# Optimization experiments

Hardware: AMD Instinct MI355X
Metric: run time of the kernel (lower is better)

The kernel has to match this reference:

```python
import jax, jax.numpy as jnp
import numpy as np

N_WORD, N_TOPIC, N_DOC = 30000, 1000, 15000
D_WORD, D_TOPIC, D_OUT = 300, 300, 128
E = dict(ww=800000, wt=400000, wd=600000, td=300000, tt=150000)
SRC_N = dict(ww=N_WORD, wt=N_WORD, wd=N_WORD, td=N_TOPIC, tt=N_TOPIC)
DST_N = dict(ww=N_WORD, wt=N_TOPIC, wd=N_DOC, td=N_DOC, tt=N_TOPIC)


def setup_inputs() -> dict:
    key = jax.random.key(0)
    ks = iter(jax.random.split(key, 64))
    inp = {}
    inp["feat_word"] = jax.random.normal(next(ks), (N_WORD, D_WORD), jnp.float32)
    inp["feat_topic"] = jax.random.normal(next(ks), (N_TOPIC, D_TOPIC), jnp.float32)
    for et in ["ww", "wt", "wd", "td", "tt"]:
        inp[f"{et}_src"] = jax.random.randint(next(ks), (E[et],), 0, SRC_N[et], jnp.int32)
        inp[f"{et}_dst"] = jax.random.randint(next(ks), (E[et],), 0, DST_N[et], jnp.int32)
        inp[f"{et}_w"] = jax.random.uniform(next(ks), (E[et],), jnp.float32)
        din = D_WORD if et[0] == "w" else D_TOPIC
        inp[f"W_{et}"] = jax.random.normal(next(ks), (din, D_OUT), jnp.float32) / np.float32(np.sqrt(din))
        inp[f"b_{et}"] = jnp.zeros((D_OUT,), jnp.float32)
    return inp


def _mean_agg(Wh, src, dst, w, n_dst):
    # DGL fn.u_mul_e('Wh','weight','m') + fn.mean('m','h'): per-edge message
    # Wh[src] * w, mean-reduced per destination node (0 for isolated nodes).
    m = Wh[src] * w[:, None]                                   # [E, D_OUT]
    s = jax.ops.segment_sum(m, dst, num_segments=n_dst)        # [n_dst, D_OUT]
    c = jax.ops.segment_sum(jnp.ones_like(w), dst, num_segments=n_dst)
    return s / jnp.maximum(c, 1.0)[:, None]


def reference(feat_word, feat_topic,
              ww_src, ww_dst, ww_w, wt_src, wt_dst, wt_w,
              wd_src, wd_dst, wd_w, td_src, td_dst, td_w,
              tt_src, tt_dst, tt_w,
              W_ww, b_ww, W_wt, b_wt, W_wd, b_wd, W_td, b_td, W_tt, b_tt):
    # NOTE: the original forward's causal/noise branch is dead code --
    # `Wh = self.weight[etype](feat_dict[srctype])` overwrites it, so the
    # live math is a plain per-edge-type linear projection of source feats.
    Wh_ww = feat_word @ W_ww + b_ww
    Wh_wt = feat_word @ W_wt + b_wt
    Wh_wd = feat_word @ W_wd + b_wd
    Wh_td = feat_topic @ W_td + b_td
    Wh_tt = feat_topic @ W_tt + b_tt
    # multi_update_all(..., 'sum'): sum the per-etype means per dst node type.
    h_word = _mean_agg(Wh_ww, ww_src, ww_dst, ww_w, N_WORD)
    h_topic = (_mean_agg(Wh_wt, wt_src, wt_dst, wt_w, N_TOPIC)
               + _mean_agg(Wh_tt, tt_src, tt_dst, tt_w, N_TOPIC))
    h_doc = (_mean_agg(Wh_wd, wd_src, wd_dst, wd_w, N_DOC)
             + _mean_agg(Wh_td, td_src, td_dst, td_w, N_DOC))
    return (h_word, h_topic, h_doc)
```

## Files before the change

kernel.cpp:

```cpp
#include <hip/hip_runtime.h>

#define N_WORD 30000
#define N_TOPIC 1000
#define N_DOC 15000
#define DIN 300
#define KP 320
#define DOUT 128

#define E_WW 800000
#define E_WT 400000
#define E_WD 600000
#define E_TD 300000
#define E_TT 150000

#define CC_WW 0
#define CC_WT 30000
#define CC_WD 31000
#define CC_TD 46000
#define CC_TT 61000
#define NBINS 62000

#define CAP_WW 80
#define CAP_WT 544
#define CAP_WD 96
#define CAP_TD 56
#define CAP_TT 240
#define SB_WW 0
#define SB_WT (SB_WW + N_WORD * CAP_WW)
#define SB_WD (SB_WT + N_TOPIC * CAP_WT)
#define SB_TD (SB_WD + N_DOC * CAP_WD)
#define SB_TT (SB_TD + N_DOC * CAP_TD)
#define SLOT_TOTAL (SB_TT + N_TOPIC * CAP_TT)

#define CNT_BLOCKS 360
#define HIST_TOTAL 4168000

#define CVT_W_CHUNKS 1200000
#define CVT_T_CHUNKS 40000
#define CVT_BLOCKS 1211
#define PREPW_BLOCKS 200

#define PFX_BLOCKS 244
#define GW_BLOCKS 469
#define GT_BLOCKS 16

#define CPAD 392

#define GB_TOPIC 250
#define GB_DOC 3750
#define GB_WORD 7500

using half8  = __attribute__((ext_vector_type(8))) _Float16;
using half2v = __attribute__((ext_vector_type(2))) _Float16;
using f32x4  = __attribute__((ext_vector_type(4))) float;

struct SegP {
    const int* src[5];
    const int* dst[5];
    const float* w[5];
};

struct WPtrs {
    const float* W[5];
    const float* b[5];
};

__device__ __forceinline__ void decode_grp(
    int b, int& ti, int& hx, int& dlo, int& bins, int& hb,
    int& ch, int& ne, int& cap, int& sbase)
{
    if (b < 64)       { ti=0; hx=b;     dlo=0;     bins=15000; hb=0;       ch=12500; ne=E_WW; cap=CAP_WW; sbase=SB_WW; }
    else if (b < 128) { ti=0; hx=b-64;  dlo=15000; bins=15000; hb=960000;  ch=12500; ne=E_WW; cap=CAP_WW; sbase=SB_WW; }
    else if (b < 192) { ti=1; hx=b-128; dlo=0;     bins=1000;  hb=1920000; ch=6250;  ne=E_WT; cap=CAP_WT; sbase=SB_WT; }
    else if (b < 288) { ti=2; hx=b-192; dlo=0;     bins=15000; hb=1984000; ch=6250;  ne=E_WD; cap=CAP_WD; sbase=SB_WD; }
    else if (b < 336) { ti=3; hx=b-288; dlo=0;     bins=15000; hb=3424000; ch=6250;  ne=E_TD; cap=CAP_TD; sbase=SB_TD; }
    else              { ti=4; hx=b-336; dlo=0;     bins=1000;  hb=4144000; ch=6250;  ne=E_TT; cap=CAP_TT; sbase=SB_TT; }
}

__device__ __forceinline__ void decode_pfx(
    int b, int& hb, int& bins, int& H, int& cb, int& tile)
{
    if (b < 59)       { hb=0;       bins=15000; H=64; cb=0;     tile=b; }
    else if (b < 118) { hb=960000;  bins=15000; H=64; cb=15000; tile=b-59; }
    else if (b < 122) { hb=1920000; bins=1000;  H=64; cb=30000; tile=b-118; }
    else if (b < 181) { hb=1984000; bins=15000; H=96; cb=31000; tile=b-122; }
    else if (b < 240) { hb=3424000; bins=15000; H=48; cb=46000; tile=b-181; }
    else              { hb=4144000; bins=1000;  H=24; cb=61000; tile=b-240; }
}

__global__ __launch_bounds__(1024) void prep_count(
    SegP S, unsigned short* __restrict__ hist,
    WPtrs WP, _Float16* __restrict__ Wt_word, _Float16* __restrict__ Wt_topic,
    float* __restrict__ bcat_word, float* __restrict__ bcat_topic,
    const float* __restrict__ feat_word, const float* __restrict__ feat_topic,
    _Float16* __restrict__ A16w, _Float16* __restrict__ A16t)
{
    __shared__ int h[15000];
    const int b = blockIdx.x;
    if (b < CNT_BLOCKS) {
        int ti, hx, dlo, bins, hb, ch, ne, cap, sbase;
        decode_grp(b, ti, hx, dlo, bins, hb, ch, ne, cap, sbase);
        (void)cap; (void)sbase;
        for (int i = threadIdx.x; i < bins; i += 1024) h[i] = 0;
        __syncthreads();
        const int* __restrict__ dst = S.dst[ti];
        int lo = hx * ch;
        int hiE = lo + ch; if (hiE > ne) hiE = ne;
        for (int i = lo + (int)threadIdx.x; i < hiE; i += 1024) {
            int ld = dst[i] - dlo;
            if ((unsigned)ld < (unsigned)bins) atomicAdd(&h[ld], 1);
        }
        __syncthreads();
        unsigned short* __restrict__ out = hist + hb + hx * bins;
        for (int i = threadIdx.x; i < bins; i += 1024)
            out[i] = (unsigned short)h[i];
    } else if (b < CNT_BLOCKS + CVT_BLOCKS) {
        int c = (b - CNT_BLOCKS) * 1024 + (int)threadIdx.x;
        if (c >= CVT_W_CHUNKS + CVT_T_CHUNKS) return;
        const float* src;
        _Float16* dstp;
        int row, k8;
        if (c < CVT_W_CHUNKS) { row = c / 40; k8 = c - row * 40; src = feat_word; dstp = A16w; }
        else { c -= CVT_W_CHUNKS; row = c / 40; k8 = c - row * 40; src = feat_topic; dstp = A16t; }
        int k = k8 * 8;
        const float* ap = src + (size_t)row * DIN + k;
        half8 hv = half8{0, 0, 0, 0, 0, 0, 0, 0};
        if (k + 8 <= DIN) {
            float4 f0 = *(const float4*)ap;
            float4 f1 = *(const float4*)(ap + 4);
            hv = half8{(_Float16)f0.x, (_Float16)f0.y, (_Float16)f0.z,
                       (_Float16)f0.w, (_Float16)f1.x, (_Float16)f1.y,
                       (_Float16)f1.z, (_Float16)f1.w};
        } else if (k < DIN) {
#pragma unroll
            for (int j = 0; j < 8; ++j)
                if (k + j < DIN) hv[j] = (_Float16)ap[j];
        }
        *(half8*)&dstp[(size_t)row * KP + k] = hv;
    } else {
        int id = (b - CNT_BLOCKS - CVT_BLOCKS) * 1024 + (int)threadIdx.x;
        const int total = (384 + 256) * KP;
        if (id >= total) return;
        int ng = id / KP;
        int k = id - ng * KP;
        int mat, n, lng;
        _Float16* Wt;
        float* bc;
        if (ng < 384) { lng = ng; mat = lng >> 7; Wt = Wt_word; bc = bcat_word; }
        else          { lng = ng - 384; mat = 3 + (lng >> 7); Wt = Wt_topic; bc = bcat_topic; }
        n = lng & 127;
        Wt[(size_t)lng * KP + k] =
            (k < DIN) ? (_Float16)WP.W[mat][(size_t)k * DOUT + n] : (_Float16)0.f;
        if (k == 0) bc[lng] = WP.b[mat][n];
    }
}

template <int NJ>
__device__ __forceinline__ void gemm16(
    const _Float16* __restrict__ A16, int M,
    const _Float16* __restrict__ Wt, const float* __restrict__ bcat,
    _Float16* __restrict__ C, int Cstride, int rowBlk,
    _Float16* __restrict__ cstage)
{
    const int t = threadIdx.x;
    const int lane = t & 63;
    const int w = t >> 6;
    const int lm = lane & 15;
    const int lq = lane >> 4;
    const int rowBase = rowBlk * 64;
    const int arow = rowBase + w * 16 + lm;

    half8 afv[10];
    if (arow < M) {
        const _Float16* ap = A16 + (size_t)arow * KP + lq * 8;
#pragma unroll
        for (int s = 0; s < 10; ++s) afv[s] = *(const half8*)(ap + s * 32);
    } else {
#pragma unroll
        for (int s = 0; s < 10; ++s) afv[s] = half8{0, 0, 0, 0, 0, 0, 0, 0};
    }

    f32x4 acc[NJ];
#pragma unroll
    for (int j = 0; j < NJ; ++j) acc[j] = f32x4{0.f, 0.f, 0.f, 0.f};

#pragma unroll
    for (int s = 0; s < 10; ++s) {
        const int k0 = s * 32 + lq * 8;
#pragma unroll
        for (int jt = 0; jt < NJ; ++jt) {
            half8 bf = *(const half8*)&Wt[(size_t)(jt * 16 + lm) * KP + k0];
            acc[jt] = __builtin_amdgcn_mfma_f32_16x16x32_f16(afv[s], bf, acc[jt], 0, 0, 0);
        }
    }

#pragma unroll
    for (int jt = 0; jt < NJ; ++jt) {
        int col = jt * 16 + lm;
        float bias = bcat[col];
#pragma unroll
        for (int reg = 0; reg < 4; ++reg) {
            int lr = w * 16 + lq * 4 + reg;
            cstage[lr * CPAD + col] = (_Float16)(acc[jt][reg] + bias);
        }
    }
    __syncthreads();

#pragma unroll
    for (int i = 0; i < NJ / 2; ++i) {
        int id = i * 256 + t;
        int row = id / (NJ * 2);
        int c8 = id - row * (NJ * 2);
        int gr = rowBase + row;
        if (gr < M)
            *(half8*)&C[(size_t)gr * Cstride + c8 * 8] =
                *(const half8*)&cstage[row * CPAD + c8 * 8];
    }
}

__global__ __launch_bounds__(256, 2) void phaseB(
    unsigned short* __restrict__ hist, int* __restrict__ cnt,
    const _Float16* __restrict__ A16w, const _Float16* __restrict__ Wtw,
    const float* __restrict__ bw, _Float16* __restrict__ Cw,
    const _Float16* __restrict__ A16t, const _Float16* __restrict__ Wtt,
    const float* __restrict__ bt, _Float16* __restrict__ Ct)
{
    __shared__ _Float16 cstage[64 * CPAD];
    const int b = blockIdx.x;
    if (b < PFX_BLOCKS) {
        int hb, bins, H, cb, tile;
        decode_pfx(b, hb, bins, H, cb, tile);
        int g = tile * 256 + (int)threadIdx.x;
        if (g < bins) {
            unsigned short* __restrict__ p = hist + hb + g;
            int run = 0;
            for (int h0 = 0; h0 < H; h0 += 8) {
                int v[8];
#pragma unroll
                for (int j = 0; j < 8; ++j) v[j] = p[(size_t)(h0 + j) * bins];
#pragma unroll
                for (int j = 0; j < 8; ++j) {
                    p[(size_t)(h0 + j) * bins] = (unsigned short)run;
                    run += v[j];
                }
            }
            cnt[cb + g] = run;
        }
    } else if (b < PFX_BLOCKS + GW_BLOCKS) {
        gemm16<24>(A16w, N_WORD, Wtw, bw, Cw, 384, b - PFX_BLOCKS, cstage);
    } else {
        gemm16<16>(A16t, N_TOPIC, Wtt, bt, Ct, 256, b - PFX_BLOCKS - GW_BLOCKS, cstage);
    }
}

__global__ __launch_bounds__(1024) void place_k(
    SegP S, const unsigned short* __restrict__ hist,
    unsigned int* __restrict__ slots)
{
    __shared__ int off[15000];
    int ti, hx, dlo, bins, hb, ch, ne, cap, sbase;
    decode_grp(blockIdx.x, ti, hx, dlo, bins, hb, ch, ne, cap, sbase);
    const unsigned short* __restrict__ po = hist + hb + hx * bins;
    for (int i = threadIdx.x; i < bins; i += 1024) off[i] = po[i];
    __syncthreads();
    const int* __restrict__ dst = S.dst[ti];
    const int* __restrict__ src = S.src[ti];
    const float* __restrict__ wp = S.w[ti];
    int lo = hx * ch;
    int hiE = lo + ch; if (hiE > ne) hiE = ne;
    for (int i = lo + (int)threadIdx.x; i < hiE; i += 1024) {
        int d = dst[i];
        int ld = d - dlo;
        if ((unsigned)ld < (unsigned)bins) {
            int pos = atomicAdd(&off[ld], 1);
            if (pos < cap) {
                unsigned short hw =
                    __builtin_bit_cast(unsigned short, (_Float16)wp[i]);
                slots[(size_t)sbase + (size_t)d * cap + pos] =
                    (unsigned int)src[i] | ((unsigned int)hw << 16);
            }
        }
    }
}

#define SV2(v, i) __builtin_shufflevector(v, v, i, i + 1)

__device__ __forceinline__ _Float16 wbits(unsigned int q)
{
    return __builtin_bit_cast(_Float16, (unsigned short)(q >> 16));
}

__device__ __forceinline__ void seg_mean16(
    const unsigned int* __restrict__ slots, int beg, int ce, int c,
    const _Float16* __restrict__ rowbase, int strideh, int ln, int sub,
    float a[8])
{
    half2v ac0 = half2v{0, 0}, ac1 = half2v{0, 0};
    half2v ac2 = half2v{0, 0}, ac3 = half2v{0, 0};
    int e = 0;
    for (; e + 16 <= ce; e += 16) {
        unsigned int q0 = slots[beg + e + 0 + sub];
        unsigned int q1 = slots[beg + e + 4 + sub];
        unsigned int q2 = slots[beg + e + 8 + sub];
        unsigned int q3 = slots[beg + e + 12 + sub];
        half8 v0 = *(const half8*)(rowbase + (size_t)(q0 & 0xFFFFu) * strideh + ln * 8);
        half8 v1 = *(const half8*)(rowbase + (size_t)(q1 & 0xFFFFu) * strideh + ln * 8);
        half8 v2 = *(const half8*)(rowbase + (size_t)(q2 & 0xFFFFu) * strideh + ln * 8);
        half8 v3 = *(const half8*)(rowbase + (size_t)(q3 & 0xFFFFu) * strideh + ln * 8);
        _Float16 h0 = wbits(q0), h1 = wbits(q1), h2 = wbits(q2), h3 = wbits(q3);
        half2v w0 = half2v{h0, h0}, w1 = half2v{h1, h1};
        half2v w2 = half2v{h2, h2}, w3 = half2v{h3, h3};
        ac0 += SV2(v0, 0) * w0 + SV2(v1, 0) * w1 + SV2(v2, 0) * w2 + SV2(v3, 0) * w3;
        ac1 += SV2(v0, 2) * w0 + SV2(v1, 2) * w1 + SV2(v2, 2) * w2 + SV2(v3, 2) * w3;
        ac2 += SV2(v0, 4) * w0 + SV2(v1, 4) * w1 + SV2(v2, 4) * w2 + SV2(v3, 4) * w3;
        ac3 += SV2(v0, 6) * w0 + SV2(v1, 6) * w1 + SV2(v2, 6) * w2 + SV2(v3, 6) * w3;
    }
    for (int e2 = e + sub; e2 < ce; e2 += 4) {
        unsigned int q = slots[beg + e2];
        half8 v = *(const half8*)(rowbase + (size_t)(q & 0xFFFFu) * strideh + ln * 8);
        _Float16 h = wbits(q);
        half2v wp = half2v{h, h};
        ac0 += SV2(v, 0) * wp;
        ac1 += SV2(v, 2) * wp;
        ac2 += SV2(v, 4) * wp;
        ac3 += SV2(v, 6) * wp;
    }
    a[0] = (float)ac0.x; a[1] = (float)ac0.y;
    a[2] = (float)ac1.x; a[3] = (float)ac1.y;
    a[4] = (float)ac2.x; a[5] = (float)ac2.y;
    a[6] = (float)ac3.x; a[7] = (float)ac3.y;
#pragma unroll
    for (int j = 0; j < 8; ++j) {
        a[j] += __shfl_down(a[j], 16);
        a[j] += __shfl_down(a[j], 32);
    }
    float inv = 1.0f / (float)(c > 1 ? c : 1);
#pragma unroll
    for (int j = 0; j < 8; ++j) a[j] *= inv;
}

__global__ __launch_bounds__(256) void gather_all(
    const unsigned int* __restrict__ slots, const int* __restrict__ cnt,
    const _Float16* __restrict__ Wh_word, const _Float16* __restrict__ Wh_topic,
    float* __restrict__ out_word, float* __restrict__ out_topic,
    float* __restrict__ out_doc)
{
    const int b = blockIdx.x;
    const int t = threadIdx.x;
    const int lane = t & 63;
    const int wv = t >> 6;
    const int sub = lane >> 4;
    const int ln = lane & 15;

    float a[8];
    float* outp;
    int node;

    if (b < GB_TOPIC) {
        node = b * 4 + wv;
        int c1 = cnt[CC_WT + node];
        int ce1 = c1 < CAP_WT ? c1 : CAP_WT;
        seg_mean16(slots, SB_WT + node * CAP_WT, ce1, c1, Wh_word + 128, 384, ln, sub, a);
        int c2 = cnt[CC_TT + node];
        int ce2 = c2 < CAP_TT ? c2 : CAP_TT;
        float a2[8];
        seg_mean16(slots, SB_TT + node * CAP_TT, ce2, c2, Wh_topic + 128, 256, ln, sub, a2);
#pragma unroll
        for (int j = 0; j < 8; ++j) a[j] += a2[j];
        outp = out_topic;
    } else if (b < GB_TOPIC + GB_DOC) {
        node = (b - GB_TOPIC) * 4 + wv;
        int c1 = cnt[CC_WD + node];
        int ce1 = c1 < CAP_WD ? c1 : CAP_WD;
        seg_mean16(slots, SB_WD + node * CAP_WD, ce1, c1, Wh_word + 256, 384, ln, sub, a);
        int c2 = cnt[CC_TD + node];
        int ce2 = c2 < CAP_TD ? c2 : CAP_TD;
        float a2[8];
        seg_mean16(slots, SB_TD + node * CAP_TD, ce2, c2, Wh_topic, 256, ln, sub, a2);
#pragma unroll
        for (int j = 0; j < 8; ++j) a[j] += a2[j];
        outp = out_doc;
    } else {
        node = (b - GB_TOPIC - GB_DOC) * 4 + wv;
        int c = cnt[CC_WW + node];
        int ce = c < CAP_WW ? c : CAP_WW;
        seg_mean16(slots, SB_WW + node * CAP_WW, ce, c, Wh_word, 384, ln, sub, a);
        outp = out_word;
    }

    if (sub == 0) {
        float4* o = (float4*)outp + (size_t)node * 32 + ln * 2;
        o[0] = make_float4(a[0], a[1], a[2], a[3]);
        o[1] = make_float4(a[4], a[5], a[6], a[7]);
    }
}

extern "C" void kernel_launch(void* const* d_in, const int* in_sizes, int n_in,
                              void* d_out, int out_size, void* d_ws, size_t ws_size,
                              hipStream_t stream)
{
    const float* feat_word  = (const float*)d_in[0];
    const float* feat_topic = (const float*)d_in[1];

    const int*   ww_src = (const int*)d_in[2];
    const int*   ww_dst = (const int*)d_in[3];
    const float* ww_w   = (const float*)d_in[4];
    const float* W_ww   = (const float*)d_in[5];
    const float* b_ww   = (const float*)d_in[6];

    const int*   wt_src = (const int*)d_in[7];
    const int*   wt_dst = (const int*)d_in[8];
    const float* wt_w   = (const float*)d_in[9];
    const float* W_wt   = (const float*)d_in[10];
    const float* b_wt   = (const float*)d_in[11];

    const int*   wd_src = (const int*)d_in[12];
    const int*   wd_dst = (const int*)d_in[13];
    const float* wd_w   = (const float*)d_in[14];
    const float* W_wd   = (const float*)d_in[15];
    const float* b_wd   = (const float*)d_in[16];

    const int*   td_src = (const int*)d_in[17];
    const int*   td_dst = (const int*)d_in[18];
    const float* td_w   = (const float*)d_in[19];
    const float* W_td   = (const float*)d_in[20];
    const float* b_td   = (const float*)d_in[21];

    const int*   tt_src = (const int*)d_in[22];
    const int*   tt_dst = (const int*)d_in[23];
    const float* tt_w   = (const float*)d_in[24];
    const float* W_tt   = (const float*)d_in[25];
    const float* b_tt   = (const float*)d_in[26];

    char* wsb = (char*)d_ws;
    size_t off = 0;
    _Float16* Wh_word  = (_Float16*)(wsb + off); off += (size_t)N_WORD * 384 * 2;
    _Float16* Wh_topic = (_Float16*)(wsb + off); off += (size_t)N_TOPIC * 256 * 2;
    _Float16* Wt_word  = (_Float16*)(wsb + off); off += (size_t)384 * KP * 2;
    _Float16* Wt_topic = (_Float16*)(wsb + off); off += (size_t)256 * KP * 2;
    float* bcat_word   = (float*)(wsb + off);    off += 384 * 4;
    float* bcat_topic  = (float*)(wsb + off);    off += 256 * 4;
    unsigned int* slots = (unsigned int*)(wsb + off); off += (size_t)SLOT_TOTAL * 4;
    int* cnt_all       = (int*)(wsb + off);      off += (size_t)NBINS * 4;
    unsigned short* hist = (unsigned short*)(wsb + off); off += (size_t)HIST_TOTAL * 2;

    _Float16* A16w = (_Float16*)slots;
    _Float16* A16t = A16w + (size_t)N_WORD * KP;

    float* out_word  = (float*)d_out;
    float* out_topic = out_word + (size_t)N_WORD * DOUT;
    float* out_doc   = out_topic + (size_t)N_TOPIC * DOUT;

    SegP S;
    S.src[0] = ww_src; S.dst[0] = ww_dst; S.w[0] = ww_w;
    S.src[1] = wt_src; S.dst[1] = wt_dst; S.w[1] = wt_w;
    S.src[2] = wd_src; S.dst[2] = wd_dst; S.w[2] = wd_w;
    S.src[3] = td_src; S.dst[3] = td_dst; S.w[3] = td_w;
    S.src[4] = tt_src; S.dst[4] = tt_dst; S.w[4] = tt_w;

    WPtrs WP;
    WP.W[0] = W_ww; WP.W[1] = W_wt; WP.W[2] = W_wd; WP.W[3] = W_td; WP.W[4] = W_tt;
    WP.b[0] = b_ww; WP.b[1] = b_wt; WP.b[2] = b_wd; WP.b[3] = b_td; WP.b[4] = b_tt;

    prep_count<<<CNT_BLOCKS + CVT_BLOCKS + PREPW_BLOCKS, 1024, 0, stream>>>(
        S, hist, WP, Wt_word, Wt_topic, bcat_word, bcat_topic,
        feat_word, feat_topic, A16w, A16t);
    phaseB<<<PFX_BLOCKS + GW_BLOCKS + GT_BLOCKS, 256, 0, stream>>>(
        hist, cnt_all,
        A16w, Wt_word, bcat_word, Wh_word,
        A16t, Wt_topic, bcat_topic, Wh_topic);
    place_k<<<CNT_BLOCKS, 1024, 0, stream>>>(S, hist, slots);
    gather_all<<<GB_TOPIC + GB_DOC + GB_WORD, 256, 0, stream>>>(
        slots, cnt_all, Wh_word, Wh_topic, out_word, out_topic, out_doc);

    (void)in_sizes; (void)n_in; (void)ws_size;
}
```

Measured before the change: 324.6 us.

## Stage A tile in LDS and split GEMM output columns across waves

The projection GEMM now stages the 64-row A tile in LDS once. Each wave computes all 64 rows for its own slice of output columns, instead of owning 16 rows across all columns. This cuts redundant global loads of the weight matrix per block and drops the LDS output staging pass. In exchange, C is written with scalar half stores rather than vectorized half8 stores. Occupancy is also raised to 3 blocks per CU through launch bounds, which risks register pressure.

Measured after the change: 289.1 us. 1.12x faster.

```diff
diff --git a/kernel.cpp b/kernel.cpp
--- a/kernel.cpp
+++ b/kernel.cpp
@@ -44,7 +44,7 @@
 #define GW_BLOCKS 469
 #define GT_BLOCKS 16
 
-#define CPAD 392
+#define PKP 328
 
 #define GB_TOPIC 250
 #define GB_DOC 3750
@@ -155,12 +155,12 @@
     }
 }
 
-template <int NJ>
-__device__ __forceinline__ void gemm16(
+template <int NJW>
+__device__ __forceinline__ void gemm_cs(
     const _Float16* __restrict__ A16, int M,
     const _Float16* __restrict__ Wt, const float* __restrict__ bcat,
     _Float16* __restrict__ C, int Cstride, int rowBlk,
-    _Float16* __restrict__ cstage)
+    _Float16* __restrict__ ldsA)
 {
     const int t = threadIdx.x;
     const int lane = t & 63;
@@ -168,64 +168,70 @@
     const int lm = lane & 15;
     const int lq = lane >> 4;
     const int rowBase = rowBlk * 64;
-    const int arow = rowBase + w * 16 + lm;
-
-    half8 afv[10];
-    if (arow < M) {
-        const _Float16* ap = A16 + (size_t)arow * KP + lq * 8;
-#pragma unroll
-        for (int s = 0; s < 10; ++s) afv[s] = *(const half8*)(ap + s * 32);
-    } else {
-#pragma unroll
-        for (int s = 0; s < 10; ++s) afv[s] = half8{0, 0, 0, 0, 0, 0, 0, 0};
-    }
-
-    f32x4 acc[NJ];
-#pragma unroll
-    for (int j = 0; j < NJ; ++j) acc[j] = f32x4{0.f, 0.f, 0.f, 0.f};
+    const int wc = w * (NJW * 16);
+
+#pragma unroll
+    for (int i = 0; i < 10; ++i) {
+        int id = i * 256 + t;
+        int row = id / 40;
+        int c8 = id - row * 40;
+        int grow = rowBase + row;
+        half8 hv = half8{0, 0, 0, 0, 0, 0, 0, 0};
+        if (grow < M) hv = *(const half8*)&A16[(size_t)grow * KP + c8 * 8];
+        *(half8*)&ldsA[row * PKP + c8 * 8] = hv;
+    }
+    __syncthreads();
+
+    f32x4 acc[4][NJW];
+#pragma unroll
+    for (int rt = 0; rt < 4; ++rt)
+#pragma unroll
+        for (int j = 0; j < NJW; ++j) acc[rt][j] = f32x4{0.f, 0.f, 0.f, 0.f};
 
 #pragma unroll
     for (int s = 0; s < 10; ++s) {
         const int k0 = s * 32 + lq * 8;
-#pragma unroll
-        for (int jt = 0; jt < NJ; ++jt) {
-            half8 bf = *(const half8*)&Wt[(size_t)(jt * 16 + lm) * KP + k0];
-            acc[jt] = __builtin_amdgcn_mfma_f32_16x16x32_f16(afv[s], bf, acc[jt], 0, 0, 0);
+        half8 bf[NJW];
+#pragma unroll
+        for (int j = 0; j < NJW; ++j)
+            bf[j] = *(const half8*)&Wt[(size_t)(wc + j * 16 + lm) * KP + k0];
+        half8 af[4];
+#pragma unroll
+        for (int rt = 0; rt < 4; ++rt)
+            af[rt] = *(const half8*)&ldsA[(rt * 16 + lm) * PKP + k0];
+#pragma unroll
+        for (int rt = 0; rt < 4; ++rt)
+#pragma unroll
+            for (int j = 0; j < NJW; ++j)
+                acc[rt][j] = __builtin_amdgcn_mfma_f32_16x16x32_f16(
+                    af[rt], bf[j], acc[rt][j], 0, 0, 0);
+    }
+
+#pragma unroll
+    for (int j = 0; j < NJW; ++j) {
+        int col = wc + j * 16 + lm;
+        float bias = bcat[col];
+#pragma unroll
+        for (int rt = 0; rt < 4; ++rt) {
+#pragma unroll
+            for (int reg = 0; reg < 4; ++reg) {
+                int gr = rowBase + rt * 16 + lq * 4 + reg;
+                if (gr < M)
+                    C[(size_t)gr * Cstride + col] =
+                        (_Float16)(acc[rt][j][reg] + bias);
+            }
         }
     }
-
-#pragma unroll
-    for (int jt = 0; jt < NJ; ++jt) {
-        int col = jt * 16 + lm;
-        float bias = bcat[col];
-#pragma unroll
-        for (int reg = 0; reg < 4; ++reg) {
-            int lr = w * 16 + lq * 4 + reg;
-            cstage[lr * CPAD + col] = (_Float16)(acc[jt][reg] + bias);
-        }
-    }
-    __syncthreads();
-
-#pragma unroll
-    for (int i = 0; i < NJ / 2; ++i) {
-        int id = i * 256 + t;
-        int row = id / (NJ * 2);
-        int c8 = id - row * (NJ * 2);
-        int gr = rowBase + row;
-        if (gr < M)
-            *(half8*)&C[(size_t)gr * Cstride + c8 * 8] =
-                *(const half8*)&cstage[row * CPAD + c8 * 8];
-    }
-}
-
-__global__ __launch_bounds__(256, 2) void phaseB(
+}
+
+__global__ __launch_bounds__(256, 3) void phaseB(
     unsigned short* __restrict__ hist, int* __restrict__ cnt,
     const _Float16* __restrict__ A16w, const _Float16* __restrict__ Wtw,
     const float* __restrict__ bw, _Float16* __restrict__ Cw,
     const _Float16* __restrict__ A16t, const _Float16* __restrict__ Wtt,
     const float* __restrict__ bt, _Float16* __restrict__ Ct)
 {
-    __shared__ _Float16 cstage[64 * CPAD];
+    __shared__ _Float16 ldsA[64 * PKP];
     const int b = blockIdx.x;
     if (b < PFX_BLOCKS) {
         int hb, bins, H, cb, tile;
@@ -247,9 +253,9 @@
             cnt[cb + g] = run;
         }
     } else if (b < PFX_BLOCKS + GW_BLOCKS) {
-        gemm16<24>(A16w, N_WORD, Wtw, bw, Cw, 384, b - PFX_BLOCKS, cstage);
+        gemm_cs<6>(A16w, N_WORD, Wtw, bw, Cw, 384, b - PFX_BLOCKS, ldsA);
     } else {
-        gemm16<16>(A16t, N_TOPIC, Wtt, bt, Ct, 256, b - PFX_BLOCKS - GW_BLOCKS, cstage);
+        gemm_cs<4>(A16t, N_TOPIC, Wtt, bt, Ct, 256, b - PFX_BLOCKS - GW_BLOCKS, ldsA);
     }
 }
 
```
